# Kernel optimization log

Hardware: AMD Instinct MI355X
Metric: run time of the kernel (lower is better)

The kernel has to match this reference:

```python
import jax, jax.numpy as jnp
import numpy as np

B = 64        # num_groups
G = 32        # group_size
D = 2000      # output dim (counts per bin/gene)
M = 16        # m_samples
E = 16        # noise_dim
DIN = 256
LAM = 1.0
TRUST = 0.25
SMOOTH = 1e-8
IPF_ITERS = 60
EPS = 1e-12


def _arch(x, noise, W, b):
    # simple linear architecture: concat(x, noise) @ W + b
    return jnp.concatenate([x, noise], axis=-1) @ W + b


def _loss(x, target, W, b, noise_loss):
    # replicate each row m times (unsqueeze(1).expand(...).reshape == repeat)
    x_rep = jnp.repeat(x, M, axis=0)                      # [n*M, DIN]
    pred = _arch(x_rep, noise_loss, W, b)                 # [n*M, D] (no act_fn in loss path)
    pred = pred.reshape(B, G, M, D).sum(axis=1)           # [B, M, D]
    term_conf = jnp.linalg.norm(pred - target[:, None, :], axis=2).mean(axis=1)  # [B]
    sq = jnp.sum(pred * pred, axis=2)                     # [B, M]
    inn = jnp.einsum('bmd,bnd->bmn', pred, pred)          # [B, M, M]
    sqd = jnp.clip(sq[:, :, None] + sq[:, None, :] - 2.0 * inn, 1e-6)
    d = jnp.sqrt(sqd)
    mask = 1.0 - jnp.eye(M, dtype=d.dtype)
    mean_pd = jnp.sum(d * mask, axis=(1, 2)) / (M * (M - 1))
    return jnp.mean(term_conf - (LAM / 2.0) * mean_pd)


def _ipf(x_pred, C):
    # KL/I-projection with row anchoring (keep_rows=True, trust_clip=0.25)
    y = jnp.clip(x_pred, 0.0)
    C = jnp.clip(C.astype(y.dtype), 0.0)
    R = y.sum(axis=2)                                     # [B, G] anchor row totals
    col_zero = (y.sum(axis=1) <= 0) & (C > 0)
    y = y + SMOOTH * col_zero[:, None, :].astype(y.dtype)
    row_zero = (y.sum(axis=2) <= 0) & (R > 0)
    y = y + SMOOTH * row_zero[:, :, None].astype(y.dtype)

    def body(_, y):
        col = jnp.clip(y.sum(axis=1), EPS)
        y = y * jnp.clip(C / col, 1.0 - TRUST, 1.0 + TRUST)[:, None, :]
        row = jnp.clip(y.sum(axis=2), EPS)
        y = y * jnp.clip(R / row, 1.0 - TRUST, 1.0 + TRUST)[:, :, None]
        return y

    y = jax.lax.fori_loop(0, IPF_ITERS, body, y)
    col = jnp.clip(y.sum(axis=1), EPS)
    return y * (C / col)[:, None, :]


def _rank(v, descending):
    # rank along last axis via double argsort (0 = first picked)
    order = jnp.argsort(-v if descending else v, axis=-1)
    return jnp.argsort(order, axis=-1)


def _round_to_targets(x, target_bd):
    # exact integerization across G per (B, D); jit-safe full-G rank replaces dynamic-k topk+scatter
    x = jnp.clip(x, 0.0)
    xf = jnp.floor(x)
    y = xf.astype(jnp.int32)                              # [B, G, D]
    frac = x - xf
    need = target_bd - y.sum(axis=1)                      # [B, D]
    pos = jnp.clip(need, 0)
    q = pos // G
    y = y + q[:, None, :]
    r = pos - q * G
    rank = _rank(jnp.transpose(frac, (0, 2, 1)), descending=True)   # [B, D, G]
    add = (rank < r[:, :, None]).astype(jnp.int32)
    y = y + jnp.transpose(add, (0, 2, 1))
    # negative residuals: remove from smallest frac among y > 0
    need = target_bd - y.sum(axis=1)
    neg = jnp.clip(-need, 0)
    neg = jnp.minimum(neg, y.sum(axis=1))
    q = neg // G
    y_before = y
    y = jnp.clip(y - q[:, None, :], 0)
    removed = (y_before - y).sum(axis=1)
    r = neg - removed
    frac_m = jnp.where(y > 0, frac, jnp.inf)
    rank = _rank(jnp.transpose(frac_m, (0, 2, 1)), descending=False)
    rem = (rank < r[:, :, None]).astype(jnp.int32)
    y = jnp.clip(y - jnp.transpose(rem, (0, 2, 1)), 0)
    return y


def setup_inputs() -> dict:
    key = jax.random.key(0)
    ks = jax.random.split(key, 6)
    x = jax.random.normal(ks[0], (B * G, DIN), dtype=jnp.float32)
    target = jax.random.uniform(ks[1], (B, D), dtype=jnp.float32) * 100.0
    target_sum = jax.random.randint(ks[2], (B, D), 0, 200, dtype=jnp.int32)
    W = jax.random.normal(ks[3], (DIN + E, D), dtype=jnp.float32) * 0.02
    b = jnp.zeros((D,), dtype=jnp.float32)
    noise_loss = jax.random.normal(ks[4], (B * G * M, E), dtype=jnp.float32)
    noise_sample = jax.random.normal(ks[5], (B * G, E), dtype=jnp.float32)
    return {"x": x, "target": target, "target_sum": target_sum, "W": W, "b": b,
            "noise_loss": noise_loss, "noise_sample": noise_sample}


def reference(x, target, target_sum, W, b, noise_loss, noise_sample):
    loss = _loss(x, target, W, b, noise_loss)
    # conditional_sample pipeline (no-grad in original): softplus act (min_value==0)
    x_pred = jax.nn.softplus(_arch(x, noise_sample, W, b)).reshape(B, G, D)
    y_float = _ipf(x_pred, target_sum.astype(jnp.float32))
    y_int = _round_to_targets(y_float, target_sum.astype(jnp.int32))
    return loss, y_int.reshape(B * G, D)
```

## Files before the change

### kernel.cpp

```cpp
#include <hip/hip_runtime.h>
#include <math.h>

#define NB   64
#define NG   32
#define ND   2000
#define NM   16
#define NE   16
#define NDIN 256
#define NK   272

__device__ __forceinline__ float clampf(float v, float lo, float hi) {
    return fminf(fmaxf(v, lo), hi);
}

__device__ __forceinline__ float softplusf(float v) {
    return (v > 20.f) ? v : log1pf(expf(v));
}

__device__ __forceinline__ float wave_sum32(float v[NG], int lane) {
    {   const bool hi = (lane & 32) != 0;
        #pragma unroll
        for (int k = 0; k < 16; ++k) {
            float s = hi ? v[k] : v[k + 16];
            float r = __shfl_xor(s, 32);
            v[k] = (hi ? v[k + 16] : v[k]) + r;
        }
    }
    {   const bool hi = (lane & 16) != 0;
        #pragma unroll
        for (int k = 0; k < 8; ++k) {
            float s = hi ? v[k] : v[k + 8];
            float r = __shfl_xor(s, 16);
            v[k] = (hi ? v[k + 8] : v[k]) + r;
        }
    }
    {   const bool hi = (lane & 8) != 0;
        #pragma unroll
        for (int k = 0; k < 4; ++k) {
            float s = hi ? v[k] : v[k + 4];
            float r = __shfl_xor(s, 8);
            v[k] = (hi ? v[k + 4] : v[k]) + r;
        }
    }
    {   const bool hi = (lane & 4) != 0;
        #pragma unroll
        for (int k = 0; k < 2; ++k) {
            float s = hi ? v[k] : v[k + 2];
            float r = __shfl_xor(s, 4);
            v[k] = (hi ? v[k + 2] : v[k]) + r;
        }
    }
    {   const bool hi = (lane & 2) != 0;
        float s = hi ? v[0] : v[1];
        float r = __shfl_xor(s, 2);
        v[0] = (hi ? v[1] : v[0]) + r;
    }
    v[0] += __shfl_xor(v[0], 1);
    return v[0];
}


__device__ __forceinline__ void ipf_path(
        const float* __restrict__ xp, const int* __restrict__ tsum,
        float* __restrict__ out, float* smem, int b, int t) {
    const int lane = t & 63, w = t >> 6;
    const int d0 = t * 4;
    const bool valid = (d0 < ND);
    const int g_own = (lane >> 1) & 31;

    float* wred = smem;

    float y0r[4][NG];
    #pragma unroll
    for (int g = 0; g < NG; ++g) {
        float4 v = make_float4(0.f, 0.f, 0.f, 0.f);
        if (valid) v = *(const float4*)(xp + (size_t)(b * NG + g) * ND + d0);
        y0r[0][g] = fmaxf(v.x, 0.f);
        y0r[1][g] = fmaxf(v.y, 0.f);
        y0r[2][g] = fmaxf(v.z, 0.f);
        y0r[3][g] = fmaxf(v.w, 0.f);
    }
    float Cc[4] = {0.f, 0.f, 0.f, 0.f};
    if (valid) {
        const int4 ci = *(const int4*)(tsum + (size_t)b * ND + d0);
        Cc[0] = (float)ci.x; Cc[1] = (float)ci.y; Cc[2] = (float)ci.z; Cc[3] = (float)ci.w;
    }
    float Ac[4] = {1.f, 1.f, 1.f, 1.f};
    float Bown = 1.f;
    float Rown;

    {
        float v[NG];
        #pragma unroll
        for (int g = 0; g < NG; ++g)
            v[g] = y0r[0][g] + y0r[1][g] + y0r[2][g] + y0r[3][g];
        const float tot = wave_sum32(v, lane);
        if ((lane & 1) == 0) wred[w * NG + g_own] = tot;
        __syncthreads();
        float s = 0.f;
        #pragma unroll
        for (int w2 = 0; w2 < 8; ++w2) s += wred[w2 * NG + g_own];
        Rown = s;
    }

    for (int q = 1; q <= 60; ++q) {
        float Bg[NG];
        #pragma unroll
        for (int g = 0; g < NG; ++g) Bg[g] = __shfl(Bown, 2 * g);
        float s0 = 0.f, s1 = 0.f, s2 = 0.f, s3 = 0.f;
        #pragma unroll
        for (int g = 0; g < NG; ++g) {
            const float bg = Bg[g];
            s0 += y0r[0][g] * bg; s1 += y0r[1][g] * bg;
            s2 += y0r[2][g] * bg; s3 += y0r[3][g] * bg;
        }
        Ac[0] *= clampf(Cc[0] / fmaxf(Ac[0] * s0, 1e-12f), 0.75f, 1.25f);
        Ac[1] *= clampf(Cc[1] / fmaxf(Ac[1] * s1, 1e-12f), 0.75f, 1.25f);
        Ac[2] *= clampf(Cc[2] / fmaxf(Ac[2] * s2, 1e-12f), 0.75f, 1.25f);
        Ac[3] *= clampf(Cc[3] / fmaxf(Ac[3] * s3, 1e-12f), 0.75f, 1.25f);
        float v[NG];
        #pragma unroll
        for (int g = 0; g < NG; ++g)
            v[g] = y0r[0][g] * Ac[0] + y0r[1][g] * Ac[1]
                 + y0r[2][g] * Ac[2] + y0r[3][g] * Ac[3];
        const float tot = wave_sum32(v, lane);
        const int buf = (q & 1) * (8 * NG);
        if ((lane & 1) == 0) wred[buf + w * NG + g_own] = tot;
        __syncthreads();
        float s = 0.f;
        #pragma unroll
        for (int w2 = 0; w2 < 8; ++w2) s += wred[buf + w2 * NG + g_own];
        Bown *= clampf(Rown / fmaxf(Bown * s, 1e-12f), 0.75f, 1.25f);
    }

    if (!valid) return;
    float Bg[NG];
    #pragma unroll
    for (int g = 0; g < NG; ++g) Bg[g] = __shfl(Bown, 2 * g);

    unsigned pk[NG];
    #pragma unroll
    for (int g = 0; g < NG; ++g) pk[g] = 0u;

    #pragma unroll
    for (int j = 0; j < 4; ++j) {
        float fr[NG];
        int   yv[NG];
        float s = 0.f;
        #pragma unroll
        for (int g = 0; g < NG; ++g) {
            const float z = y0r[j][g] * Ac[j] * Bg[g];
            fr[g] = z;
            s += z;
        }
        const float F = Cc[j] / fmaxf(s, 1e-12f);
        int isum = 0;
        #pragma unroll
        for (int g = 0; g < NG; ++g) {
            const float y = fr[g] * F;
            const float fl = floorf(y);
            yv[g] = (int)fl;
            fr[g] = y - fl;
            isum += yv[g];
        }
        const int Ci = (int)Cc[j];
        const int need = Ci - isum;
        const int pos = max(need, 0);
        const int q = pos >> 5;
        const int r = pos & 31;
        #pragma unroll
        for (int g = 0; g < NG; ++g) yv[g] += q;
        #pragma unroll
        for (int g = 0; g < NG; ++g) {
            int rank = 0;
            #pragma unroll
            for (int h = 0; h < NG; ++h) {
                if (h == g) continue;
                rank += (h < g) ? (fr[h] >= fr[g] ? 1 : 0) : (fr[h] > fr[g] ? 1 : 0);
            }
            if (rank < r) yv[g] += 1;
        }
        int neg = max(-need, 0);
        neg = min(neg, isum + pos);
        if (neg > 0) {
            const int q2 = neg >> 5;
            int removed = 0;
            unsigned elig = 0u;
            #pragma unroll
            for (int g = 0; g < NG; ++g) {
                const int yb = yv[g];
                const int yn = max(yb - q2, 0);
                removed += yb - yn;
                yv[g] = yn;
                if (yn > 0) elig |= (1u << g);
            }
            int r2 = neg - removed;
            for (; r2 > 0; --r2) {
                float best = __builtin_inff();
                int bi = -1;
                #pragma unroll
                for (int g = 0; g < NG; ++g) {
                    const float fm = ((elig >> g) & 1u) ? fr[g] : __builtin_inff();
                    if (fm < best) { best = fm; bi = g; }
                }
                if (bi < 0) break;
                elig &= ~(1u << bi);
                yv[bi] = max(yv[bi] - 1, 0);
            }
        }
        #pragma unroll
        for (int g = 0; g < NG; ++g)
            pk[g] |= ((unsigned)yv[g]) << (8 * j);
    }
    #pragma unroll
    for (int g = 0; g < NG; ++g) {
        float* op = &out[1 + (size_t)(b * NG + g) * ND + d0];
        op[0] = (float)(pk[g] & 0xffu);
        op[1] = (float)((pk[g] >> 8) & 0xffu);
        op[2] = (float)((pk[g] >> 16) & 0xffu);
        op[3] = (float)((pk[g] >> 24) & 0xffu);
    }
}

__device__ __forceinline__ void loss_path(
        const float* __restrict__ x, const float* __restrict__ nl,
        const float* __restrict__ tgt, const float* __restrict__ W,
        const float* __restrict__ bias, float* __restrict__ res2,
        float* smem, int cx, int b, int t) {
    float* xsl = smem;
    float* nsl = smem + 256;
    float* tgl = smem + 512;
    float* pt  = smem + 764;

    if (t < 256) {
        const float* xb = x + (size_t)b * NG * NDIN;
        float s = 0.f;
        for (int g = 0; g < NG; ++g) s += xb[g * NDIN + t];
        xsl[t] = s;
        const float* nb = nl + (size_t)b * NG * (NM * NE);
        float s2 = 0.f;
        for (int g = 0; g < NG; ++g) s2 += nb[g * (NM * NE) + t];
        nsl[t] = s2;
    }

    int tm = 0, tn = 0;
    if (t >= 16 && t < 152) {
        int p = t - 16;
        for (int m = 0; m < NM; ++m) {
            int c = NM - m;
            if (p < c) { tm = m; tn = m + p; break; }
            p -= c;
        }
    }
    __syncthreads();

    const int d = cx * 250 + t;
    if (t < 250) {
        tgl[t] = tgt[b * ND + d];
        float xw = 0.f;
        #pragma unroll 8
        for (int k = 0; k < NDIN; ++k) xw += xsl[k] * W[(size_t)k * ND + d];
        float we[NE];
        #pragma unroll
        for (int e = 0; e < NE; ++e) we[e] = W[(size_t)(NDIN + e) * ND + d];
        const float base0 = xw + (float)NG * bias[d];
        #pragma unroll
        for (int m = 0; m < NM; ++m) {
            float pm = base0;
            #pragma unroll
            for (int e = 0; e < NE; ++e) pm += nsl[m * NE + e] * we[e];
            pt[m * 252 + t] = pm;
        }
    }
    if (t < 32) {
        pt[(t >> 1) * 252 + 250 + (t & 1)] = 0.f;
        if (t < 2) tgl[250 + t] = 0.f;
    }
    __syncthreads();

    float acc = 0.f;
    if (t < 16) {
        const float4* pa  = (const float4*)&pt[t * 252];
        const float4* tga = (const float4*)&tgl[0];
        for (int i = 0; i < 63; ++i) {
            float4 pv = pa[i], tv = tga[i];
            float e0 = pv.x - tv.x, e1 = pv.y - tv.y, e2 = pv.z - tv.z, e3 = pv.w - tv.w;
            acc += e0 * e0 + e1 * e1 + e2 * e2 + e3 * e3;
        }
    } else if (t < 152) {
        const float4* pa = (const float4*)&pt[tm * 252];
        const float4* pb = (const float4*)&pt[tn * 252];
        for (int i = 0; i < 63; ++i) {
            float4 u = pa[i], v = pb[i];
            acc += u.x * v.x + u.y * v.y + u.z * v.z + u.w * v.w;
        }
    }
    if (t < 152) res2[((size_t)b * 8 + cx) * 152 + t] = acc;
}

extern "C" __global__ __launch_bounds__(512)
void mega(const float* __restrict__ x, const float* __restrict__ nl,
          const float* __restrict__ tgt, const float* __restrict__ W,
          const float* __restrict__ bias, const float* __restrict__ xp,
          const int* __restrict__ tsum, float* __restrict__ out,
          float* __restrict__ res2) {
    __shared__ float smem[4800];
    const int bid = blockIdx.x;
    const int t = threadIdx.x;
    if (bid < NB) {
        ipf_path(xp, tsum, out, smem, bid, t);
    } else {
        const int q = bid - NB;
        loss_path(x, nl, tgt, W, bias, res2, smem, q & 7, q >> 3, t);
    }
}

extern "C" __global__ __launch_bounds__(64)
void k2b_combine(const float* __restrict__ res2, float* __restrict__ out) {
    const int b = blockIdx.x, t = threadIdx.x;
    __shared__ float res[152];
    for (int tau = t; tau < 152; tau += 64) {
        float s = 0.f;
        #pragma unroll
        for (int c = 0; c < 8; ++c) s += res2[((size_t)b * 8 + c) * 152 + tau];
        res[tau] = s;
    }
    __syncthreads();
    if (t == 0) {
        float conf = 0.f;
        for (int m = 0; m < NM; ++m) conf += sqrtf(res[m]);
        conf *= (1.f / NM);
        float pd = 0.f;
        for (int m = 0; m < NM; ++m) {
            const int offm = 16 + m * NM - m * (m - 1) / 2;
            const float sqm = res[offm];
            for (int n = m + 1; n < NM; ++n) {
                const int offn = 16 + n * NM - n * (n - 1) / 2;
                const float sqn = res[offn];
                const float inn = res[offm + (n - m)];
                pd += sqrtf(fmaxf(sqm + sqn - 2.f * inn, 1e-6f));
            }
        }
        pd = 2.f * pd / (float)(NM * (NM - 1));
        atomicAdd(out, (conf - 0.5f * pd) * (1.f / NB));
    }
}

extern "C" __global__ __launch_bounds__(256)
void k3_xpred(const float* __restrict__ x, const float* __restrict__ nsamp,
              const float* __restrict__ W, const float* __restrict__ bias,
              float* __restrict__ xp) {
    const int dx = blockIdx.x;
    const int rb = blockIdx.y;
    const int t  = threadIdx.x;
    __shared__ float xr[8][NK];
    #pragma unroll
    for (int r = 0; r < 8; ++r) {
        const int row = rb * 8 + r;
        xr[r][t] = x[(size_t)row * NDIN + t];
        if (t < NE) xr[r][NDIN + t] = nsamp[row * NE + t];
    }
    __syncthreads();
    if (t >= 250) return;
    const int d = dx * 500 + 2 * t;
    float acc[8][2];
    #pragma unroll
    for (int r = 0; r < 8; ++r) { acc[r][0] = 0.f; acc[r][1] = 0.f; }
    for (int k = 0; k < NK; k += 4) {
        float2 w[4];
        #pragma unroll
        for (int kk = 0; kk < 4; ++kk) w[kk] = *(const float2*)&W[(size_t)(k + kk) * ND + d];
        #pragma unroll
        for (int r = 0; r < 8; ++r) {
            const float4 xv = *(const float4*)&xr[r][k];
            acc[r][0] += xv.x * w[0].x + xv.y * w[1].x + xv.z * w[2].x + xv.w * w[3].x;
            acc[r][1] += xv.x * w[0].y + xv.y * w[1].y + xv.z * w[2].y + xv.w * w[3].y;
        }
    }
    const float2 bv = *(const float2*)&bias[d];
    #pragma unroll
    for (int r = 0; r < 8; ++r) {
        float2 o;
        o.x = softplusf(acc[r][0] + bv.x);
        o.y = softplusf(acc[r][1] + bv.y);
        *(float2*)&xp[(size_t)(rb * 8 + r) * ND + d] = o;
    }
}

extern "C" void kernel_launch(void* const* d_in, const int* in_sizes, int n_in,
                              void* d_out, int out_size, void* d_ws, size_t ws_size,
                              hipStream_t stream) {
    const float* x     = (const float*)d_in[0];
    const float* tgt   = (const float*)d_in[1];
    const int*   tsum  = (const int*)d_in[2];
    const float* W     = (const float*)d_in[3];
    const float* bias  = (const float*)d_in[4];
    const float* nl    = (const float*)d_in[5];
    const float* nsamp = (const float*)d_in[6];
    float* out = (float*)d_out;
    float* xp  = (float*)d_ws;

    (void)in_sizes; (void)n_in; (void)out_size; (void)ws_size;

    const size_t XPB = (size_t)2048 * 2000 * 4;
    float* res2 = (float*)((char*)d_ws + XPB);

    hipMemsetAsync(d_out, 0, sizeof(float), stream);

    hipLaunchKernelGGL(k3_xpred, dim3(4, 256), dim3(256), 0, stream,
                       x, nsamp, W, bias, xp);
    hipLaunchKernelGGL(mega, dim3(NB + 512), dim3(512), 0, stream,
                       x, nl, tgt, W, bias, xp, tsum, out, res2);
    hipLaunchKernelGGL(k2b_combine, dim3(NB), dim3(64), 0, stream, res2, out);
}
```

Baseline: 318.7 us.

## Double IPF block width to two columns per thread; widen xpred to four columns

The IPF blocks now use 1024 threads with each thread owning two columns instead of four. This halves the per-thread serial work and register load in the 60-iteration loop, at the cost of reducing partial sums across 16 waves instead of 8. Loss-path blocks launch with 1024 threads but exit the extra half immediately. The xpred GEMM kernel is changed separately so each thread computes four columns with float4 loads, halving its grid and raising reuse of the shared activation rows.

```diff
diff --git a/kernel.cpp b/kernel.cpp
--- a/kernel.cpp
+++ b/kernel.cpp
@@ -64,42 +64,39 @@
         const float* __restrict__ xp, const int* __restrict__ tsum,
         float* __restrict__ out, float* smem, int b, int t) {
     const int lane = t & 63, w = t >> 6;
-    const int d0 = t * 4;
+    const int d0 = t * 2;
     const bool valid = (d0 < ND);
     const int g_own = (lane >> 1) & 31;
 
     float* wred = smem;
 
-    float y0r[4][NG];
+    float y0r[2][NG];
     #pragma unroll
     for (int g = 0; g < NG; ++g) {
-        float4 v = make_float4(0.f, 0.f, 0.f, 0.f);
-        if (valid) v = *(const float4*)(xp + (size_t)(b * NG + g) * ND + d0);
+        float2 v = make_float2(0.f, 0.f);
+        if (valid) v = *(const float2*)(xp + (size_t)(b * NG + g) * ND + d0);
         y0r[0][g] = fmaxf(v.x, 0.f);
         y0r[1][g] = fmaxf(v.y, 0.f);
-        y0r[2][g] = fmaxf(v.z, 0.f);
-        y0r[3][g] = fmaxf(v.w, 0.f);
-    }
-    float Cc[4] = {0.f, 0.f, 0.f, 0.f};
+    }
+    float Cc[2] = {0.f, 0.f};
     if (valid) {
-        const int4 ci = *(const int4*)(tsum + (size_t)b * ND + d0);
-        Cc[0] = (float)ci.x; Cc[1] = (float)ci.y; Cc[2] = (float)ci.z; Cc[3] = (float)ci.w;
-    }
-    float Ac[4] = {1.f, 1.f, 1.f, 1.f};
+        const int2 ci = *(const int2*)(tsum + (size_t)b * ND + d0);
+        Cc[0] = (float)ci.x; Cc[1] = (float)ci.y;
+    }
+    float Ac[2] = {1.f, 1.f};
     float Bown = 1.f;
     float Rown;
 
     {
         float v[NG];
         #pragma unroll
-        for (int g = 0; g < NG; ++g)
-            v[g] = y0r[0][g] + y0r[1][g] + y0r[2][g] + y0r[3][g];
+        for (int g = 0; g < NG; ++g) v[g] = y0r[0][g] + y0r[1][g];
         const float tot = wave_sum32(v, lane);
         if ((lane & 1) == 0) wred[w * NG + g_own] = tot;
         __syncthreads();
         float s = 0.f;
         #pragma unroll
-        for (int w2 = 0; w2 < 8; ++w2) s += wred[w2 * NG + g_own];
+        for (int w2 = 0; w2 < 16; ++w2) s += wred[w2 * NG + g_own];
         Rown = s;
     }
 
@@ -107,29 +104,26 @@
         float Bg[NG];
         #pragma unroll
         for (int g = 0; g < NG; ++g) Bg[g] = __shfl(Bown, 2 * g);
-        float s0 = 0.f, s1 = 0.f, s2 = 0.f, s3 = 0.f;
+        float s0 = 0.f, s1 = 0.f;
         #pragma unroll
         for (int g = 0; g < NG; ++g) {
             const float bg = Bg[g];
-            s0 += y0r[0][g] * bg; s1 += y0r[1][g] * bg;
-            s2 += y0r[2][g] * bg; s3 += y0r[3][g] * bg;
+            s0 += y0r[0][g] * bg;
+            s1 += y0r[1][g] * bg;
         }
         Ac[0] *= clampf(Cc[0] / fmaxf(Ac[0] * s0, 1e-12f), 0.75f, 1.25f);
         Ac[1] *= clampf(Cc[1] / fmaxf(Ac[1] * s1, 1e-12f), 0.75f, 1.25f);
-        Ac[2] *= clampf(Cc[2] / fmaxf(Ac[2] * s2, 1e-12f), 0.75f, 1.25f);
-        Ac[3] *= clampf(Cc[3] / fmaxf(Ac[3] * s3, 1e-12f), 0.75f, 1.25f);
         float v[NG];
         #pragma unroll
         for (int g = 0; g < NG; ++g)
-            v[g] = y0r[0][g] * Ac[0] + y0r[1][g] * Ac[1]
-                 + y0r[2][g] * Ac[2] + y0r[3][g] * Ac[3];
+            v[g] = y0r[0][g] * Ac[0] + y0r[1][g] * Ac[1];
         const float tot = wave_sum32(v, lane);
-        const int buf = (q & 1) * (8 * NG);
+        const int buf = (q & 1) * (16 * NG);
         if ((lane & 1) == 0) wred[buf + w * NG + g_own] = tot;
         __syncthreads();
         float s = 0.f;
         #pragma unroll
-        for (int w2 = 0; w2 < 8; ++w2) s += wred[buf + w2 * NG + g_own];
+        for (int w2 = 0; w2 < 16; ++w2) s += wred[buf + w2 * NG + g_own];
         Bown *= clampf(Rown / fmaxf(Bown * s, 1e-12f), 0.75f, 1.25f);
     }
 
@@ -138,12 +132,8 @@
     #pragma unroll
     for (int g = 0; g < NG; ++g) Bg[g] = __shfl(Bown, 2 * g);
 
-    unsigned pk[NG];
-    #pragma unroll
-    for (int g = 0; g < NG; ++g) pk[g] = 0u;
-
-    #pragma unroll
-    for (int j = 0; j < 4; ++j) {
+    #pragma unroll
+    for (int j = 0; j < 2; ++j) {
         float fr[NG];
         int   yv[NG];
         float s = 0.f;
@@ -210,15 +200,7 @@
         }
         #pragma unroll
         for (int g = 0; g < NG; ++g)
-            pk[g] |= ((unsigned)yv[g]) << (8 * j);
-    }
-    #pragma unroll
-    for (int g = 0; g < NG; ++g) {
-        float* op = &out[1 + (size_t)(b * NG + g) * ND + d0];
-        op[0] = (float)(pk[g] & 0xffu);
-        op[1] = (float)((pk[g] >> 8) & 0xffu);
-        op[2] = (float)((pk[g] >> 16) & 0xffu);
-        op[3] = (float)((pk[g] >> 24) & 0xffu);
+            out[1 + (size_t)(b * NG + g) * ND + (d0 + j)] = (float)yv[g];
     }
 }
 
@@ -298,7 +280,7 @@
     if (t < 152) res2[((size_t)b * 8 + cx) * 152 + t] = acc;
 }
 
-extern "C" __global__ __launch_bounds__(512)
+extern "C" __global__ __launch_bounds__(1024)
 void mega(const float* __restrict__ x, const float* __restrict__ nl,
           const float* __restrict__ tgt, const float* __restrict__ W,
           const float* __restrict__ bias, const float* __restrict__ xp,
@@ -310,6 +292,7 @@
     if (bid < NB) {
         ipf_path(xp, tsum, out, smem, bid, t);
     } else {
+        if (t >= 512) return;
         const int q = bid - NB;
         loss_path(x, nl, tgt, W, bias, res2, smem, q & 7, q >> 3, t);
     }
@@ -362,28 +345,34 @@
     }
     __syncthreads();
     if (t >= 250) return;
-    const int d = dx * 500 + 2 * t;
-    float acc[8][2];
-    #pragma unroll
-    for (int r = 0; r < 8; ++r) { acc[r][0] = 0.f; acc[r][1] = 0.f; }
+    const int d = dx * 1000 + 4 * t;
+    float acc[8][4];
+    #pragma unroll
+    for (int r = 0; r < 8; ++r) {
+        acc[r][0] = 0.f; acc[r][1] = 0.f; acc[r][2] = 0.f; acc[r][3] = 0.f;
+    }
     for (int k = 0; k < NK; k += 4) {
-        float2 w[4];
-        #pragma unroll
-        for (int kk = 0; kk < 4; ++kk) w[kk] = *(const float2*)&W[(size_t)(k + kk) * ND + d];
+        float4 w[4];
+        #pragma unroll
+        for (int kk = 0; kk < 4; ++kk) w[kk] = *(const float4*)&W[(size_t)(k + kk) * ND + d];
         #pragma unroll
         for (int r = 0; r < 8; ++r) {
             const float4 xv = *(const float4*)&xr[r][k];
             acc[r][0] += xv.x * w[0].x + xv.y * w[1].x + xv.z * w[2].x + xv.w * w[3].x;
             acc[r][1] += xv.x * w[0].y + xv.y * w[1].y + xv.z * w[2].y + xv.w * w[3].y;
-        }
-    }
-    const float2 bv = *(const float2*)&bias[d];
+            acc[r][2] += xv.x * w[0].z + xv.y * w[1].z + xv.z * w[2].z + xv.w * w[3].z;
+            acc[r][3] += xv.x * w[0].w + xv.y * w[1].w + xv.z * w[2].w + xv.w * w[3].w;
+        }
+    }
+    const float4 bv = *(const float4*)&bias[d];
     #pragma unroll
     for (int r = 0; r < 8; ++r) {
-        float2 o;
+        float4 o;
         o.x = softplusf(acc[r][0] + bv.x);
         o.y = softplusf(acc[r][1] + bv.y);
-        *(float2*)&xp[(size_t)(rb * 8 + r) * ND + d] = o;
+        o.z = softplusf(acc[r][2] + bv.z);
+        o.w = softplusf(acc[r][3] + bv.w);
+        *(float4*)&xp[(size_t)(rb * 8 + r) * ND + d] = o;
     }
 }
 
@@ -407,9 +396,9 @@
 
     hipMemsetAsync(d_out, 0, sizeof(float), stream);
 
-    hipLaunchKernelGGL(k3_xpred, dim3(4, 256), dim3(256), 0, stream,
+    hipLaunchKernelGGL(k3_xpred, dim3(2, 256), dim3(256), 0, stream,
                        x, nsamp, W, bias, xp);
-    hipLaunchKernelGGL(mega, dim3(NB + 512), dim3(512), 0, stream,
+    hipLaunchKernelGGL(mega, dim3(NB + 512), dim3(1024), 0, stream,
                        x, nl, tgt, W, bias, xp, tsum, out, res2);
     hipLaunchKernelGGL(k2b_combine, dim3(NB), dim3(64), 0, stream, res2, out);
 }
```

New measurement: 514.2 us. +61.4%, slower.
